# Performance work log

Measured on AMD Instinct MI355X. Metric: run time of the kernel, lower is better.

Reference implementation:

```python
import jax, jax.numpy as jnp
import numpy as np


def setup_inputs() -> dict:
    key = jax.random.key(0)
    k1, k2 = jax.random.split(key)
    B, HW, C = 256, 196, 384
    x = jax.random.normal(k1, (B, HW + 1, C), dtype=jnp.float32)
    edge_aggregation = jax.random.normal(k2, (B, HW, C), dtype=jnp.float32)
    return {"x": x, "edge_aggregation": edge_aggregation}


def reference(x, edge_aggregation):
    # x: (B, HW+1, C); edge_aggregation: (B, HW, C)
    nodes = x[:, 1:]                                    # (B, HW, C)
    # AvgPool1d over full HW length == mean over token axis
    ea = jnp.mean(edge_aggregation, axis=1, keepdims=True)   # (B, 1, C)
    channel_importance = jax.nn.sigmoid(ea)                  # (B, 1, C)
    # nodes @ channel_importance^T -> (B, HW, 1); keep as (B, HW)
    channel_aggregation = jnp.einsum('bnc,bc->bn', nodes, channel_importance[:, 0])
    # ascending sort indices per sample (matches torch.sort default)
    idx = jnp.argsort(channel_aggregation, axis=1)           # (B, HW)
    nodes_sorted = jnp.take_along_axis(nodes, idx[:, :, None], axis=1)  # (B, HW, C)
    HW = nodes.shape[1]
    start = HW // 4 * 3                                       # keep top quartile
    nodes_pooled = nodes_sorted[:, start:]                    # (B, HW - start, C)
    out = jnp.concatenate([x[:, :1], nodes_pooled], axis=1)   # (B, HW-start+1, C)
    return out
```

## Files before the change

### kernel.cpp

```cpp
#include <hip/hip_runtime.h>
#include <math.h>

#define NB      256
#define NNODES  196
#define NC      384
#define SEQ     197
#define START   147
#define KEEP    49
#define OUTROWS 50
#define C4      96

#define NT      960
#define P1T     576
#define P1RG    6
#define SROWS   88
#define SITERS  22

__global__ __launch_bounds__(NT)
void pool_fused(const float* __restrict__ x,
                const float* __restrict__ ea,
                float* __restrict__ out) {
    __shared__ alignas(16) float stage[SROWS][NC];
    __shared__ float partial[P1RG][NC];
    __shared__ alignas(16) float imp[NC];
    __shared__ float sc[NNODES];
    __shared__ int   sel[KEEP];

    const int b    = blockIdx.x;
    const int tid  = threadIdx.x;
    const int wave = tid >> 6;
    const int lane = tid & 63;
    const float* nodes = x + ((size_t)b * SEQ + 1) * NC;

    if (tid < P1T) {
        const int rg = tid / C4;
        const int c4 = tid % C4;
        const float4* p = (const float4*)(ea + (size_t)b * NNODES * NC) + c4;
        double ax = 0.0, ay = 0.0, az = 0.0, aw = 0.0;
        for (int row = rg; row < NNODES; row += P1RG) {
            float4 v = p[(size_t)row * C4];
            ax += v.x; ay += v.y; az += v.z; aw += v.w;
        }
        partial[rg][4 * c4 + 0] = (float)ax;
        partial[rg][4 * c4 + 1] = (float)ay;
        partial[rg][4 * c4 + 2] = (float)az;
        partial[rg][4 * c4 + 3] = (float)aw;
    } else {
        const int t = tid - P1T;
        const float4* src = (const float4*)nodes;
        float4* dst = (float4*)&stage[0][0];
        #pragma unroll
        for (int i = 0; i < SITERS; ++i)
            dst[t + 384 * i] = src[t + 384 * i];
    }
    __syncthreads();

    if (tid < NC) {
        double s = 0.0;
        #pragma unroll
        for (int rg = 0; rg < P1RG; ++rg) s += (double)partial[rg][tid];
        float m = (float)(s * (1.0 / (double)NNODES));
        imp[tid] = 1.0f / (1.0f + expf(-m));
    }
    __syncthreads();

    {
        const float2* imp2 = (const float2*)imp;
        float2 w[3];
        #pragma unroll
        for (int j = 0; j < 3; ++j) w[j] = imp2[lane + 64 * j];

        for (int n = wave; n < NNODES; n += 15) {
            double acc = 0.0;
            if (n < SROWS) {
                const float2* row2 = (const float2*)&stage[n][0];
                #pragma unroll
                for (int j = 0; j < 3; ++j) {
                    float2 v = row2[lane + 64 * j];
                    acc += (double)v.x * (double)w[j].x + (double)v.y * (double)w[j].y;
                }
            } else {
                const float2* row2 = (const float2*)(nodes + (size_t)n * NC);
                #pragma unroll
                for (int j = 0; j < 3; ++j) {
                    float2 v = row2[lane + 64 * j];
                    acc += (double)v.x * (double)w[j].x + (double)v.y * (double)w[j].y;
                }
            }
            #pragma unroll
            for (int off = 32; off > 0; off >>= 1)
                acc += __shfl_xor(acc, off);
            if (lane == 0) sc[n] = (float)acc;
        }
    }
    __syncthreads();

    if (tid < NNODES) {
        const float s = sc[tid];
        int rank = 0;
        for (int m = 0; m < NNODES; ++m) {
            const float sm = sc[m];
            rank += (sm < s) || (sm == s && m < tid);
        }
        if (rank >= START) sel[rank - START] = tid;
    }
    __syncthreads();

    {
        const int jg = tid / C4;
        const int c4 = tid % C4;
        const float4* nodes4 = (const float4*)nodes;
        const float4* cls4   = (const float4*)(x + (size_t)b * SEQ * NC);
        float4* out4         = (float4*)(out + (size_t)b * OUTROWS * NC);
        #pragma unroll
        for (int it = 0; it < 5; ++it) {
            int j = jg + 10 * it;
            float4 v;
            if (j == 0) {
                v = cls4[c4];
            } else {
                int n = sel[j - 1];
                v = (n < SROWS) ? ((const float4*)&stage[n][0])[c4]
                                : nodes4[(size_t)n * C4 + c4];
            }
            out4[(size_t)j * C4 + c4] = v;
        }
    }
}

extern "C" void kernel_launch(void* const* d_in, const int* in_sizes, int n_in,
                              void* d_out, int out_size, void* d_ws, size_t ws_size,
                              hipStream_t stream) {
    const float* x  = (const float*)d_in[0];
    const float* ea = (const float*)d_in[1];
    float* out      = (float*)d_out;

    hipLaunchKernelGGL(pool_fused, dim3(NB), dim3(NT), 0, stream, x, ea, out);
}
```

Measured before the change: 40.49 us.

## Stage node rows via direct global-to-LDS loads and use all threads for mean reduction

Replaces the register-mediated staging copy of the first 88 node rows with `global_load_lds` DMA instructions issued by every thread, so the data goes straight into shared memory. With staging no longer tying up a dedicated thread subset, all 960 threads now split the edge-aggregation column reduction into 10 row groups instead of 6. The aim is more memory requests in flight and less register and VALU pressure during the bandwidth-bound first phase. It relies on the compiler emitting the right waits before the barrier for the async LDS writes.

```diff
diff --git a/kernel.cpp b/kernel.cpp
--- a/kernel.cpp
+++ b/kernel.cpp
@@ -11,17 +11,21 @@
 #define C4      96
 
 #define NT      960
-#define P1T     576
-#define P1RG    6
+#define RG      10
 #define SROWS   88
-#define SITERS  22
+#define SF4     (SROWS * C4)
+
+#define GLOAD_LDS(gptr, lptr)                                                  \
+    __builtin_amdgcn_global_load_lds(                                          \
+        (const __attribute__((address_space(1))) void*)(gptr),                 \
+        (__attribute__((address_space(3))) void*)(lptr), 16, 0, 0)
 
 __global__ __launch_bounds__(NT)
-void pool_fused(const float* __restrict__ x,
-                const float* __restrict__ ea,
-                float* __restrict__ out) {
+void pool_dma(const float* __restrict__ x,
+              const float* __restrict__ ea,
+              float* __restrict__ out) {
     __shared__ alignas(16) float stage[SROWS][NC];
-    __shared__ float partial[P1RG][NC];
+    __shared__ float partial[RG][NC];
     __shared__ alignas(16) float imp[NC];
     __shared__ float sc[NNODES];
     __shared__ int   sel[KEEP];
@@ -32,33 +36,36 @@
     const int lane = tid & 63;
     const float* nodes = x + ((size_t)b * SEQ + 1) * NC;
 
-    if (tid < P1T) {
+    {
+        const float4* gsrc = (const float4*)nodes;
+        float4* lbase = (float4*)&stage[0][0];
+        #pragma unroll
+        for (int i = 0; i < 8; ++i)
+            GLOAD_LDS(gsrc + tid + 960 * i, lbase + tid + 960 * i);
+        if (tid < SF4 - 7680)
+            GLOAD_LDS(gsrc + tid + 7680, lbase + tid + 7680);
+    }
+
+    {
         const int rg = tid / C4;
         const int c4 = tid % C4;
-        const float4* p = (const float4*)(ea + (size_t)b * NNODES * NC) + c4;
+        const float4* p = (const float4*)(ea + (size_t)b * NNODES * NC);
         double ax = 0.0, ay = 0.0, az = 0.0, aw = 0.0;
-        for (int row = rg; row < NNODES; row += P1RG) {
-            float4 v = p[(size_t)row * C4];
+        for (int row = rg; row < NNODES; row += RG) {
+            float4 v = p[(size_t)row * C4 + c4];
             ax += v.x; ay += v.y; az += v.z; aw += v.w;
         }
         partial[rg][4 * c4 + 0] = (float)ax;
         partial[rg][4 * c4 + 1] = (float)ay;
         partial[rg][4 * c4 + 2] = (float)az;
         partial[rg][4 * c4 + 3] = (float)aw;
-    } else {
-        const int t = tid - P1T;
-        const float4* src = (const float4*)nodes;
-        float4* dst = (float4*)&stage[0][0];
-        #pragma unroll
-        for (int i = 0; i < SITERS; ++i)
-            dst[t + 384 * i] = src[t + 384 * i];
     }
     __syncthreads();
 
     if (tid < NC) {
         double s = 0.0;
         #pragma unroll
-        for (int rg = 0; rg < P1RG; ++rg) s += (double)partial[rg][tid];
+        for (int rg = 0; rg < RG; ++rg) s += (double)partial[rg][tid];
         float m = (float)(s * (1.0 / (double)NNODES));
         imp[tid] = 1.0f / (1.0f + expf(-m));
     }
@@ -135,5 +142,5 @@
     const float* ea = (const float*)d_in[1];
     float* out      = (float*)d_out;
 
-    hipLaunchKernelGGL(pool_fused, dim3(NB), dim3(NT), 0, stream, x, ea, out);
+    hipLaunchKernelGGL(pool_dma, dim3(NB), dim3(NT), 0, stream, x, ea, out);
 }
```

Measured after the change: 39.91 us. Within noise of the previous version (-1.4%).
